# Optimization experiments

Measured on AMD Instinct MI355X. Metric: run time of the kernel, lower is better.

The kernel has to match this reference:

```python
import jax, jax.numpy as jnp
import numpy as np

BS, N, M, D = 8, 2048, 64, 1024
N_WAY, N_SHOT = 64, 5


def setup_inputs() -> dict:
    key = jax.random.key(0)
    k1, k2, k3, k4, k5 = jax.random.split(key, 5)
    return {
        "prototypes": jax.random.normal(k1, (BS, M, D), dtype=jnp.float32),
        "masktypes": jax.random.uniform(k2, (BS, M, D), dtype=jnp.float32),
        "query": jax.random.normal(k3, (BS, N, D), dtype=jnp.float32),
        "support": jax.random.normal(k4, (BS, N_WAY * N_SHOT, D), dtype=jnp.float32),
        "support_labels": jax.random.randint(k5, (BS, N_WAY * N_SHOT), 0, N_WAY, dtype=jnp.int64),
        "scale": jnp.ones((1,), dtype=jnp.float32),
        "n_way": N_WAY,
        "n_shot": N_SHOT,
    }


def reference(prototypes, masktypes, query, support, support_labels, scale, n_way, n_shot):
    # Masked squared Euclidean distance:
    #   logits[b,n,m] = sum_d (mask[b,m,d] * (query[b,n,d] - proto[b,m,d]))^2
    # Expanded via the GEMM trick to avoid the (bs,n,m,d) intermediate:
    #   = sum_d mask^2 q^2 - 2 sum_d q (mask^2 p) + sum_d (mask p)^2
    dims = prototypes.shape[-1]
    mask2 = masktypes * masktypes                       # [b,m,d]
    q_term = jnp.einsum('bnd,bmd->bnm', query * query, mask2)
    cross = jnp.einsum('bnd,bmd->bnm', query, mask2 * prototypes)
    mp = masktypes * prototypes                         # [b,m,d]
    p_term = jnp.sum(mp * mp, axis=-1)[:, None, :]      # [b,1,m]
    logits = (q_term - 2.0 * cross + p_term) / dims     # normalize=True
    return scale * logits
```

## Files before the change

kernel.cpp:

```cpp
#include <hip/hip_runtime.h>

#define BSZ 8
#define NQ 2048
#define MP 64
#define DD 1024
#define K2ALL 2048
#define BN 16
#define LDKQ 2056
#define NSTEP 64
#define NTILES (NQ / BN)

typedef __bf16 bf16x8 __attribute__((ext_vector_type(8)));
typedef float f32x4 __attribute__((ext_vector_type(4)));
typedef unsigned short us8 __attribute__((ext_vector_type(8)));

__device__ __forceinline__ unsigned short f2bf(float f) {
    union { float f; unsigned int u; } v; v.f = f;
    unsigned int u = v.u;
    return (unsigned short)((u + 0x7FFFu + ((u >> 16) & 1u)) >> 16);
}

__global__ __launch_bounds__(256) void pack_kernel(
    const float* __restrict__ proto,
    const float* __restrict__ mask,
    unsigned short* __restrict__ Pf,
    float* __restrict__ Pterm)
{
    const int row = blockIdx.x;
    const int m = row & 63;
    const int b = row >> 6;
    const int t = threadIdx.x;

    const float4 mk = *(const float4*)(mask  + (size_t)row * DD + 4 * t);
    const float4 pr = *(const float4*)(proto + (size_t)row * DD + 4 * t);

    const float m2x = mk.x * mk.x, m2y = mk.y * mk.y,
                m2z = mk.z * mk.z, m2w = mk.w * mk.w;
    const float ax = mk.x * pr.x, ay = mk.y * pr.y,
                az = mk.z * pr.z, aw = mk.w * pr.w;
    float pacc = ax * ax + ay * ay + az * az + aw * aw;

    us8 o;
    o[0] = f2bf(m2x); o[1] = f2bf(-2.f * m2x * pr.x);
    o[2] = f2bf(m2y); o[3] = f2bf(-2.f * m2y * pr.y);
    o[4] = f2bf(m2z); o[5] = f2bf(-2.f * m2z * pr.z);
    o[6] = f2bf(m2w); o[7] = f2bf(-2.f * m2w * pr.w);

    const int mt   = m >> 4;
    const int s    = t >> 2;
    const int lane = (t & 3) * 16 + (m & 15);
    const size_t idx = ((((size_t)(b * 4 + mt)) * 64 + s) * 64 + lane) * 8;
    *(us8*)(Pf + idx) = o;

    __shared__ float red[4];
    #pragma unroll
    for (int off = 32; off > 0; off >>= 1)
        pacc += __shfl_down(pacc, off, 64);
    const int lane64 = t & 63, w = t >> 6;
    if (lane64 == 0) red[w] = pacc;
    __syncthreads();
    if (t == 0) Pterm[row] = red[0] + red[1] + red[2] + red[3];
}

__global__ __launch_bounds__(256) void proto_main_kernel(
    const float* __restrict__ query,
    const unsigned short* __restrict__ Pf,
    const float* __restrict__ Pterm,
    const float* __restrict__ scale,
    float* __restrict__ out)
{
    __shared__ unsigned short Qs[BN][LDKQ];

    const int tid = threadIdx.x;
    const int bid = blockIdx.x;
    const int b  = bid & 7;
    const int n0 = (bid >> 3) * BN;

    const int qrow = tid >> 4;
    const int qc   = tid & 15;
    const float* qptr = query + ((size_t)b * NQ + n0 + qrow) * DD + 4 * qc;

    const int lane = tid & 63;
    const int wid  = tid >> 6;
    const int lrow = lane & 15;
    const int lq   = (lane >> 4) * 8;

    const int mcol = 16 * wid + lrow;
    const unsigned short* bbase =
        Pf + (((size_t)(b * 4 + wid)) * 64) * 512 + (size_t)lane * 8;

    float4 qv[16];
    #pragma unroll
    for (int p = 0; p < 16; ++p)
        qv[p] = *(const float4*)(qptr + 64 * p);

    const float pt = Pterm[b * MP + mcol];
    const float sc = scale[0] * (1.0f / (float)DD);

    #pragma unroll
    for (int p = 0; p < 16; ++p) {
        const float4 q = qv[p];
        us8 o;
        o[0] = f2bf(q.x * q.x); o[1] = f2bf(q.x);
        o[2] = f2bf(q.y * q.y); o[3] = f2bf(q.y);
        o[4] = f2bf(q.z * q.z); o[5] = f2bf(q.z);
        o[6] = f2bf(q.w * q.w); o[7] = f2bf(q.w);
        *(us8*)(&Qs[qrow][8 * qc + 128 * p]) = o;
    }
    __syncthreads();

    f32x4 acc = (f32x4){0.f, 0.f, 0.f, 0.f};
    bf16x8 bq[8];
    #pragma unroll
    for (int i = 0; i < 8; ++i)
        bq[i] = *(const bf16x8*)(bbase + (size_t)i * 512);

    #pragma unroll
    for (int g = 0; g < NSTEP; g += 8) {
        #pragma unroll
        for (int j = 0; j < 8; ++j) {
            const bf16x8 bb = bq[j];
            if (g + 8 + j < NSTEP)
                bq[j] = *(const bf16x8*)(bbase + (size_t)(g + 8 + j) * 512);
            const bf16x8 a = *(const bf16x8*)(&Qs[lrow][32 * (g + j) + lq]);
            acc = __builtin_amdgcn_mfma_f32_16x16x32_bf16(a, bb, acc, 0, 0, 0);
        }
    }

    const size_t ob = ((size_t)b * NQ + (size_t)(n0 + (lane >> 4) * 4)) * MP + mcol;
    #pragma unroll
    for (int r = 0; r < 4; ++r)
        out[ob + (size_t)r * MP] = (acc[r] + pt) * sc;
}

extern "C" void kernel_launch(void* const* d_in, const int* in_sizes, int n_in,
                              void* d_out, int out_size, void* d_ws, size_t ws_size,
                              hipStream_t stream) {
    (void)in_sizes; (void)n_in; (void)ws_size; (void)out_size;
    const float* proto = (const float*)d_in[0];
    const float* mask  = (const float*)d_in[1];
    const float* query = (const float*)d_in[2];
    const float* scale = (const float*)d_in[5];
    float* out = (float*)d_out;

    unsigned short* Pf = (unsigned short*)d_ws;
    float* Pterm = (float*)((char*)d_ws + (size_t)BSZ * MP * K2ALL * 2);

    pack_kernel<<<dim3(BSZ * MP), dim3(256), 0, stream>>>(proto, mask, Pf, Pterm);
    proto_main_kernel<<<dim3(BSZ * NTILES), dim3(256), 0, stream>>>(
        query, Pf, Pterm, scale, out);
}
```

Before: 123.2 us.

## Pipeline query load/convert with MFMA over four K chunks

Splits the query tile's K dimension into four chunks, each with its own LDS slice. The global load and bf16 conversion of later chunks now overlap with MFMA work on earlier chunks, instead of loading and converting the whole tile before any compute starts. This lowers peak register use for the query staging, since only 8 float4 are live instead of 16. The cost is extra __syncthreads barriers and a chunked LDS layout with new padding.

```diff
diff --git a/kernel.cpp b/kernel.cpp
--- a/kernel.cpp
+++ b/kernel.cpp
@@ -6,9 +6,9 @@
 #define DD 1024
 #define K2ALL 2048
 #define BN 16
-#define LDKQ 2056
 #define NSTEP 64
 #define NTILES (NQ / BN)
+#define LDC 520
 
 typedef __bf16 bf16x8 __attribute__((ext_vector_type(8)));
 typedef float f32x4 __attribute__((ext_vector_type(4)));
@@ -69,7 +69,7 @@
     const float* __restrict__ scale,
     float* __restrict__ out)
 {
-    __shared__ unsigned short Qs[BN][LDKQ];
+    __shared__ unsigned short Qs[4][BN][LDC];
 
     const int tid = threadIdx.x;
     const int bid = blockIdx.x;
@@ -89,43 +89,64 @@
     const unsigned short* bbase =
         Pf + (((size_t)(b * 4 + wid)) * 64) * 512 + (size_t)lane * 8;
 
-    float4 qv[16];
-    #pragma unroll
-    for (int p = 0; p < 16; ++p)
-        qv[p] = *(const float4*)(qptr + 64 * p);
-
     const float pt = Pterm[b * MP + mcol];
     const float sc = scale[0] * (1.0f / (float)DD);
 
-    #pragma unroll
-    for (int p = 0; p < 16; ++p) {
-        const float4 q = qv[p];
-        us8 o;
-        o[0] = f2bf(q.x * q.x); o[1] = f2bf(q.x);
-        o[2] = f2bf(q.y * q.y); o[3] = f2bf(q.y);
-        o[4] = f2bf(q.z * q.z); o[5] = f2bf(q.z);
-        o[6] = f2bf(q.w * q.w); o[7] = f2bf(q.w);
-        *(us8*)(&Qs[qrow][8 * qc + 128 * p]) = o;
+#define LOADQ(r0, r1, r2, r3, C)                                         \
+    r0 = *(const float4*)(qptr + 256 * (C));                             \
+    r1 = *(const float4*)(qptr + 256 * (C) + 64);                        \
+    r2 = *(const float4*)(qptr + 256 * (C) + 128);                       \
+    r3 = *(const float4*)(qptr + 256 * (C) + 192);
+
+#define CV1(Q, C, PP) {                                                  \
+    us8 o;                                                               \
+    o[0] = f2bf(Q.x * Q.x); o[1] = f2bf(Q.x);                            \
+    o[2] = f2bf(Q.y * Q.y); o[3] = f2bf(Q.y);                            \
+    o[4] = f2bf(Q.z * Q.z); o[5] = f2bf(Q.z);                            \
+    o[6] = f2bf(Q.w * Q.w); o[7] = f2bf(Q.w);                            \
+    *(us8*)(&Qs[C][qrow][8 * qc + 128 * (PP)]) = o; }
+
+#define CV4(r0, r1, r2, r3, C)                                           \
+    CV1(r0, C, 0) CV1(r1, C, 1) CV1(r2, C, 2) CV1(r3, C, 3)
+
+#define MFMA_CHUNK(C)                                                    \
+    _Pragma("unroll")                                                    \
+    for (int s = 0; s < 16; ++s) {                                       \
+        const int t = 16 * (C) + s;                                      \
+        const bf16x8 bb = bq[t & 7];                                     \
+        if (t + 8 < NSTEP)                                               \
+            bq[t & 7] = *(const bf16x8*)(bbase + (size_t)(t + 8) * 512); \
+        const bf16x8 a = *(const bf16x8*)(&Qs[C][lrow][32 * s + lq]);    \
+        acc = __builtin_amdgcn_mfma_f32_16x16x32_bf16(a, bb, acc, 0, 0, 0); \
     }
-    __syncthreads();
 
+    float4 ra0, ra1, ra2, ra3, rb0, rb1, rb2, rb3;
     f32x4 acc = (f32x4){0.f, 0.f, 0.f, 0.f};
     bf16x8 bq[8];
+
+    LOADQ(ra0, ra1, ra2, ra3, 0)
+    LOADQ(rb0, rb1, rb2, rb3, 1)
     #pragma unroll
     for (int i = 0; i < 8; ++i)
         bq[i] = *(const bf16x8*)(bbase + (size_t)i * 512);
+    CV4(ra0, ra1, ra2, ra3, 0)
+    __syncthreads();
 
-    #pragma unroll
-    for (int g = 0; g < NSTEP; g += 8) {
-        #pragma unroll
-        for (int j = 0; j < 8; ++j) {
-            const bf16x8 bb = bq[j];
-            if (g + 8 + j < NSTEP)
-                bq[j] = *(const bf16x8*)(bbase + (size_t)(g + 8 + j) * 512);
-            const bf16x8 a = *(const bf16x8*)(&Qs[lrow][32 * (g + j) + lq]);
-            acc = __builtin_amdgcn_mfma_f32_16x16x32_bf16(a, bb, acc, 0, 0, 0);
-        }
-    }
+    LOADQ(ra0, ra1, ra2, ra3, 2)
+    CV4(rb0, rb1, rb2, rb3, 1)
+    MFMA_CHUNK(0)
+    __syncthreads();
+
+    LOADQ(rb0, rb1, rb2, rb3, 3)
+    CV4(ra0, ra1, ra2, ra3, 2)
+    MFMA_CHUNK(1)
+    __syncthreads();
+
+    CV4(rb0, rb1, rb2, rb3, 3)
+    MFMA_CHUNK(2)
+    __syncthreads();
+
+    MFMA_CHUNK(3)
 
     const size_t ob = ((size_t)b * NQ + (size_t)(n0 + (lane >> 4) * 4)) * MP + mcol;
     #pragma unroll
```

Result: slower. 126.8 us (+2.9%).
